# Kernel tuning notes

Hardware: AMD Instinct MI355X
Metric: run time of the kernel (lower is better)

## Reference

```python
import jax, jax.numpy as jnp
import numpy as np

B, T, H, U = 64, 4096, 256, 256


def setup_inputs() -> dict:
    key = jax.random.key(0)
    ks = jax.random.split(key, 8)
    s = 1.0 / np.sqrt(H)
    return {
        "query": jax.random.normal(ks[0], (B, H), dtype=jnp.float32),
        "values": jax.random.normal(ks[1], (B, T, H), dtype=jnp.float32),
        "W1": jax.random.normal(ks[2], (H, U), dtype=jnp.float32) * s,
        "b1": jnp.zeros((U,), dtype=jnp.float32),
        "W2": jax.random.normal(ks[3], (H, U), dtype=jnp.float32) * s,
        "b2": jnp.zeros((U,), dtype=jnp.float32),
        "V": jax.random.normal(ks[4], (U, 1), dtype=jnp.float32) * (1.0 / np.sqrt(U)),
        "bV": jnp.zeros((1,), dtype=jnp.float32),
    }


def reference(query, values, W1, b1, W2, b2, V, bV):
    # query: [B,H] -> [B,1,U]; values: [B,T,H] -> [B,T,U]
    q_proj = (query @ W1 + b1)[:, None, :]            # [B,1,U]
    v_proj = jnp.einsum('bth,hu->btu', values, W2) + b2  # [B,T,U]
    score = jnp.tanh(q_proj + v_proj) @ V + bV        # [B,T,1]
    attention_weights = jax.nn.softmax(score, axis=1)  # softmax over T
    context_vector = jnp.sum(attention_weights * values, axis=1)  # [B,H]
    return context_vector, attention_weights
```

## Files before the change

### kernel.cpp

```cpp
#include <hip/hip_runtime.h>
#include <stdint.h>

#define B_ 64
#define T_ 4096
#define H_ 256
#define U_ 256

typedef float f32x4 __attribute__((ext_vector_type(4)));
typedef short short8 __attribute__((ext_vector_type(8)));

__device__ __forceinline__ short bf16rne(float f) {
    uint32_t x = __builtin_bit_cast(uint32_t, f);
    return (short)((x + 0x7FFFu + ((x >> 16) & 1u)) >> 16);
}

__device__ __forceinline__ float fast_tanh(float x) {
    float e = __expf(2.0f * x);
    return 1.0f - 2.0f * __builtin_amdgcn_rcpf(e + 1.0f);
}

__global__ __launch_bounds__(256) void k_prep(const float* __restrict__ W2,
                                              uint16_t* __restrict__ w2t,
                                              const float* __restrict__ query,
                                              const float* __restrict__ W1,
                                              const float* __restrict__ b1,
                                              const float* __restrict__ b2,
                                              float* __restrict__ qpc) {
    if (blockIdx.x < 256) {
        int idx = blockIdx.x * 256 + threadIdx.x;
        int h = idx >> 8;
        int u = idx & 255;
        w2t[u * 256 + h] = (uint16_t)bf16rne(W2[idx]);
    } else {
        __shared__ float qrow[H_];
        int b = blockIdx.x - 256, u = threadIdx.x;
        qrow[u] = query[b * H_ + u];
        __syncthreads();
        float acc = b1[u] + b2[u];
#pragma unroll 8
        for (int h = 0; h < H_; ++h) acc += qrow[h] * W1[h * U_ + u];
        qpc[b * U_ + u] = acc;
    }
}

#define TR 32
#define NT 8
__global__ __launch_bounds__(512, 2) void k_main(const float* __restrict__ values,
                                                 const uint16_t* __restrict__ w2t,
                                                 const float* __restrict__ qpc,
                                                 const float* __restrict__ V,
                                                 float* __restrict__ score,
                                                 float* __restrict__ part_O,
                                                 float* __restrict__ part_s) {
    __shared__ __align__(16) char Ab[TR * 512];
    __shared__ float red[TR][9];
    __shared__ float Ored[TR][16][16];
    __shared__ float sred[TR];

    const int tid = threadIdx.x;
    const int wg = blockIdx.x;
    const int b = wg >> 4;
    const int chunk = (wg & 15) * (NT * TR);

    const int w = tid >> 6;
    const int l = tid & 63;
    const int c = l & 15;
    const int g = l >> 4;

    short8 afr[2][8];
#pragma unroll
    for (int s = 0; s < 2; ++s) {
        const uint16_t* ap = w2t + (size_t)(w * 32 + s * 16 + c) * 256 + g * 8;
#pragma unroll
        for (int ks = 0; ks < 8; ++ks) afr[s][ks] = *(const short8*)(ap + ks * 32);
    }
    float qv[2][4], vv[2][4];
#pragma unroll
    for (int s = 0; s < 2; ++s)
#pragma unroll
        for (int r = 0; r < 4; ++r) {
            int u = w * 32 + s * 16 + g * 4 + r;
            qv[s][r] = qpc[b * U_ + u];
            vv[s][r] = V[u];
        }

    const float* vbase = values + (size_t)b * T_ * H_;
    const int srow = tid >> 4;
    const int q = tid & 15;
    const int sswz = (srow & 7) << 4;
    char* wr0 = Ab + srow * 512 + ((q * 16) ^ sswz);
    char* wr1 = Ab + srow * 512 + ((q * 16 + 256) ^ sswz);
    const float* sbase = vbase + (size_t)srow * H_ + q * 8;

    f32x4 vt[3][4];
    float Oacc[16];
#pragma unroll
    for (int j = 0; j < 16; ++j) Oacc[j] = 0.f;
    float sacc = 0.f;

    {
        const float* nb0 = sbase + (size_t)chunk * H_;
        vt[0][0] = *(const f32x4*)(nb0);       vt[0][1] = *(const f32x4*)(nb0 + 4);
        vt[0][2] = *(const f32x4*)(nb0 + 128); vt[0][3] = *(const f32x4*)(nb0 + 132);
        const float* nb1 = sbase + (size_t)(chunk + TR) * H_;
        vt[1][0] = *(const f32x4*)(nb1);       vt[1][1] = *(const f32x4*)(nb1 + 4);
        vt[1][2] = *(const f32x4*)(nb1 + 128); vt[1][3] = *(const f32x4*)(nb1 + 132);
    }

#pragma unroll
    for (int t = 0; t < NT; ++t) {
        const int cs = t % 3;
        const int os = (t + 2) % 3;
        __syncthreads();
        {
            short8 s0, s1;
            s0[0] = bf16rne(vt[cs][0][0]); s0[1] = bf16rne(vt[cs][0][1]);
            s0[2] = bf16rne(vt[cs][0][2]); s0[3] = bf16rne(vt[cs][0][3]);
            s0[4] = bf16rne(vt[cs][1][0]); s0[5] = bf16rne(vt[cs][1][1]);
            s0[6] = bf16rne(vt[cs][1][2]); s0[7] = bf16rne(vt[cs][1][3]);
            s1[0] = bf16rne(vt[cs][2][0]); s1[1] = bf16rne(vt[cs][2][1]);
            s1[2] = bf16rne(vt[cs][2][2]); s1[3] = bf16rne(vt[cs][2][3]);
            s1[4] = bf16rne(vt[cs][3][0]); s1[5] = bf16rne(vt[cs][3][1]);
            s1[6] = bf16rne(vt[cs][3][2]); s1[7] = bf16rne(vt[cs][3][3]);
            *(short8*)wr0 = s0;
            *(short8*)wr1 = s1;
        }
        if (t > 0) {
            float ssum = 0.f;
#pragma unroll
            for (int j = 0; j < 8; ++j) ssum += red[srow][j];
            float wgt = __expf(ssum);
            if (q == 0) {
                sacc += wgt;
                score[(size_t)b * T_ + chunk + (t - 1) * TR + srow] = ssum;
            }
#pragma unroll
            for (int vj = 0; vj < 4; ++vj)
#pragma unroll
                for (int j = 0; j < 4; ++j)
                    Oacc[vj * 4 + j] += wgt * vt[os][vj][j];
        }
        if (t + 2 < NT) {
            const float* nb = sbase + (size_t)(chunk + (t + 2) * TR) * H_;
            vt[os][0] = *(const f32x4*)(nb);       vt[os][1] = *(const f32x4*)(nb + 4);
            vt[os][2] = *(const f32x4*)(nb + 128); vt[os][3] = *(const f32x4*)(nb + 132);
        }
        __syncthreads();
#pragma unroll
        for (int sub = 0; sub < 2; ++sub) {
            const char* rp = Ab + (sub * 16 + c) * 512;
            const int swz = (c & 7) << 4;
            f32x4 acc0 = (f32x4)(0.0f);
            f32x4 acc1 = (f32x4)(0.0f);
#pragma unroll
            for (int ks = 0; ks < 8; ++ks) {
                short8 bf = *(const short8*)(rp + ((ks * 64 + g * 16) ^ swz));
                acc0 = __builtin_amdgcn_mfma_f32_16x16x32_bf16(afr[0][ks], bf, acc0, 0, 0, 0);
                acc1 = __builtin_amdgcn_mfma_f32_16x16x32_bf16(afr[1][ks], bf, acc1, 0, 0, 0);
            }
            float p = 0.f;
#pragma unroll
            for (int r = 0; r < 4; ++r) {
                p += fast_tanh(acc0[r] + qv[0][r]) * vv[0][r];
                p += fast_tanh(acc1[r] + qv[1][r]) * vv[1][r];
            }
            p += __shfl_xor(p, 16, 64);
            p += __shfl_xor(p, 32, 64);
            if (g == 0) red[sub * 16 + c][w] = p;
        }
    }
    __syncthreads();
    {
        const int fs = (NT - 1) % 3;
        float ssum = 0.f;
#pragma unroll
        for (int j = 0; j < 8; ++j) ssum += red[srow][j];
        float wgt = __expf(ssum);
        if (q == 0) {
            sacc += wgt;
            score[(size_t)b * T_ + chunk + (NT - 1) * TR + srow] = ssum;
        }
#pragma unroll
        for (int vj = 0; vj < 4; ++vj)
#pragma unroll
            for (int j = 0; j < 4; ++j)
                Oacc[vj * 4 + j] += wgt * vt[fs][vj][j];
    }
#pragma unroll
    for (int j = 0; j < 16; ++j) Ored[srow][q][j] = Oacc[j];
    if (q == 0) sred[srow] = sacc;
    __syncthreads();
    if (tid < 256) {
        int col = tid;
        int qq, jj;
        if (col < 128) { qq = col >> 3; jj = col & 7; }
        else           { qq = (col - 128) >> 3; jj = 8 + (col & 7); }
        float o = 0.f;
#pragma unroll
        for (int s = 0; s < TR; ++s) o += Ored[s][qq][jj];
        part_O[(size_t)wg * 256 + col] = o;
    }
    if (tid == 0) {
        float sb = 0.f;
#pragma unroll
        for (int s = 0; s < TR; ++s) sb += sred[s];
        part_s[wg] = sb;
    }
}

__global__ __launch_bounds__(256) void k_fin(const float* __restrict__ part_O,
                                             const float* __restrict__ part_s,
                                             const float* __restrict__ score,
                                             float* __restrict__ ctx,
                                             float* __restrict__ weights) {
    int b = blockIdx.x;
    int col = threadIdx.x;
    float sb = 0.f;
#pragma unroll
    for (int ch = 0; ch < 16; ++ch) sb += part_s[b * 16 + ch];
    float o = 0.f;
#pragma unroll
    for (int ch = 0; ch < 16; ++ch) o += part_O[(size_t)(b * 16 + ch) * 256 + col];
    float inv = 1.0f / sb;
    ctx[b * H_ + col] = o * inv;
#pragma unroll
    for (int i = 0; i < 16; ++i) {
        float s = score[(size_t)b * T_ + col + i * 256];
        weights[(size_t)b * T_ + col + i * 256] = __expf(s) * inv;
    }
}

extern "C" void kernel_launch(void* const* d_in, const int* in_sizes, int n_in,
                              void* d_out, int out_size, void* d_ws, size_t ws_size,
                              hipStream_t stream) {
    const float* query  = (const float*)d_in[0];
    const float* values = (const float*)d_in[1];
    const float* W1     = (const float*)d_in[2];
    const float* b1     = (const float*)d_in[3];
    const float* W2     = (const float*)d_in[4];
    const float* b2     = (const float*)d_in[5];
    const float* V      = (const float*)d_in[6];

    float* out = (float*)d_out;
    float* ctx = out;
    float* weights = out + B_ * H_;

    char* ws = (char*)d_ws;
    uint16_t* w2t   = (uint16_t*)ws;
    float* qpc      = (float*)(ws + 131072);
    float* scorebuf = (float*)(ws + 131072 + 65536);
    float* part_O   = (float*)(ws + 131072 + 65536 + 1048576);
    float* part_s   = (float*)(ws + 131072 + 65536 + 2097152);

    k_prep<<<dim3(320), dim3(256), 0, stream>>>(W2, w2t, query, W1, b1, b2, qpc);
    k_main<<<dim3(1024), dim3(512), 0, stream>>>(values, w2t, qpc, V, scorebuf,
                                                 part_O, part_s);
    k_fin<<<dim3(64), dim3(256), 0, stream>>>(part_O, part_s, scorebuf, ctx, weights);
}
```

Measured before the change: 93.42 us.

## Double-buffer LDS tiles, remap value loads per wave, widen finalize grid

Measured after the change: 126.7 us. 35.6% more time.

```diff
diff --git a/kernel.cpp b/kernel.cpp
--- a/kernel.cpp
+++ b/kernel.cpp
@@ -8,6 +8,7 @@
 
 typedef float f32x4 __attribute__((ext_vector_type(4)));
 typedef short short8 __attribute__((ext_vector_type(8)));
+typedef short short4v __attribute__((ext_vector_type(4)));
 
 __device__ __forceinline__ short bf16rne(float f) {
     uint32_t x = __builtin_bit_cast(uint32_t, f);
@@ -52,10 +53,10 @@
                                                  float* __restrict__ score,
                                                  float* __restrict__ part_O,
                                                  float* __restrict__ part_s) {
-    __shared__ __align__(16) char Ab[TR * 512];
-    __shared__ float red[TR][9];
-    __shared__ float Ored[TR][16][16];
-    __shared__ float sred[TR];
+    __shared__ __align__(16) char Ab[2][TR * 512];
+    __shared__ float red[2][TR][12];
+    __shared__ float Ored[8][256];
+    __shared__ float sred[8];
 
     const int tid = threadIdx.x;
     const int wg = blockIdx.x;
@@ -84,71 +85,71 @@
             vv[s][r] = V[u];
         }
 
-    const float* vbase = values + (size_t)b * T_ * H_;
-    const int srow = tid >> 4;
-    const int q = tid & 15;
-    const int sswz = (srow & 7) << 4;
-    char* wr0 = Ab + srow * 512 + ((q * 16) ^ sswz);
-    char* wr1 = Ab + srow * 512 + ((q * 16 + 256) ^ sswz);
-    const float* sbase = vbase + (size_t)srow * H_ + q * 8;
+    const float* vbase = values + (size_t)b * T_ * H_ + (size_t)chunk * H_;
+    const int sswz = (l * 8) ^ (w << 4);
 
     f32x4 vt[3][4];
-    float Oacc[16];
-#pragma unroll
-    for (int j = 0; j < 16; ++j) Oacc[j] = 0.f;
+    float Oacc[4] = {0.f, 0.f, 0.f, 0.f};
     float sacc = 0.f;
 
-    {
-        const float* nb0 = sbase + (size_t)chunk * H_;
-        vt[0][0] = *(const f32x4*)(nb0);       vt[0][1] = *(const f32x4*)(nb0 + 4);
-        vt[0][2] = *(const f32x4*)(nb0 + 128); vt[0][3] = *(const f32x4*)(nb0 + 132);
-        const float* nb1 = sbase + (size_t)(chunk + TR) * H_;
-        vt[1][0] = *(const f32x4*)(nb1);       vt[1][1] = *(const f32x4*)(nb1 + 4);
-        vt[1][2] = *(const f32x4*)(nb1 + 128); vt[1][3] = *(const f32x4*)(nb1 + 132);
+#pragma unroll
+    for (int j = 0; j < 4; ++j) {
+        vt[0][j] = *(const f32x4*)(vbase + j * 2048 + w * 256 + l * 4);
+        vt[1][j] = *(const f32x4*)(vbase + 8192 + j * 2048 + w * 256 + l * 4);
+    }
+#pragma unroll
+    for (int j = 0; j < 4; ++j) {
+        short4v s4;
+        s4[0] = bf16rne(vt[0][j][0]); s4[1] = bf16rne(vt[0][j][1]);
+        s4[2] = bf16rne(vt[0][j][2]); s4[3] = bf16rne(vt[0][j][3]);
+        *(short4v*)(Ab[0] + (j * 8 + w) * 512 + sswz) = s4;
     }
 
 #pragma unroll
     for (int t = 0; t < NT; ++t) {
-        const int cs = t % 3;
-        const int os = (t + 2) % 3;
         __syncthreads();
-        {
-            short8 s0, s1;
-            s0[0] = bf16rne(vt[cs][0][0]); s0[1] = bf16rne(vt[cs][0][1]);
-            s0[2] = bf16rne(vt[cs][0][2]); s0[3] = bf16rne(vt[cs][0][3]);
-            s0[4] = bf16rne(vt[cs][1][0]); s0[5] = bf16rne(vt[cs][1][1]);
-            s0[6] = bf16rne(vt[cs][1][2]); s0[7] = bf16rne(vt[cs][1][3]);
-            s1[0] = bf16rne(vt[cs][2][0]); s1[1] = bf16rne(vt[cs][2][1]);
-            s1[2] = bf16rne(vt[cs][2][2]); s1[3] = bf16rne(vt[cs][2][3]);
-            s1[4] = bf16rne(vt[cs][3][0]); s1[5] = bf16rne(vt[cs][3][1]);
-            s1[6] = bf16rne(vt[cs][3][2]); s1[7] = bf16rne(vt[cs][3][3]);
-            *(short8*)wr0 = s0;
-            *(short8*)wr1 = s1;
-        }
         if (t > 0) {
-            float ssum = 0.f;
-#pragma unroll
-            for (int j = 0; j < 8; ++j) ssum += red[srow][j];
-            float wgt = __expf(ssum);
-            if (q == 0) {
-                sacc += wgt;
-                score[(size_t)b * T_ + chunk + (t - 1) * TR + srow] = ssum;
-            }
-#pragma unroll
-            for (int vj = 0; vj < 4; ++vj)
-#pragma unroll
-                for (int j = 0; j < 4; ++j)
-                    Oacc[vj * 4 + j] += wgt * vt[os][vj][j];
+            const int os = (t + 2) % 3;
+            float p = 0.f;
+            if (l < 4) {
+                const float* rr = &red[(t - 1) & 1][l * 8 + w][0];
+                f32x4 r0 = *(const f32x4*)(rr);
+                f32x4 r1 = *(const f32x4*)(rr + 4);
+                float ssum = (r0[0] + r0[1] + r0[2] + r0[3]) +
+                             (r1[0] + r1[1] + r1[2] + r1[3]);
+                p = __expf(ssum);
+                sacc += p;
+                score[(size_t)b * T_ + chunk + (t - 1) * TR + l * 8 + w] = ssum;
+            }
+#pragma unroll
+            for (int j = 0; j < 4; ++j) {
+                float wgt = __shfl(p, j, 64);
+                Oacc[0] += wgt * vt[os][j][0];
+                Oacc[1] += wgt * vt[os][j][1];
+                Oacc[2] += wgt * vt[os][j][2];
+                Oacc[3] += wgt * vt[os][j][3];
+            }
         }
         if (t + 2 < NT) {
-            const float* nb = sbase + (size_t)(chunk + (t + 2) * TR) * H_;
-            vt[os][0] = *(const f32x4*)(nb);       vt[os][1] = *(const f32x4*)(nb + 4);
-            vt[os][2] = *(const f32x4*)(nb + 128); vt[os][3] = *(const f32x4*)(nb + 132);
-        }
-        __syncthreads();
+            const int ns = (t + 2) % 3;
+            const float* nb = vbase + (size_t)(t + 2) * 8192;
+#pragma unroll
+            for (int j = 0; j < 4; ++j)
+                vt[ns][j] = *(const f32x4*)(nb + j * 2048 + w * 256 + l * 4);
+        }
+        if (t + 1 < NT) {
+            const int cs = (t + 1) % 3;
+#pragma unroll
+            for (int j = 0; j < 4; ++j) {
+                short4v s4;
+                s4[0] = bf16rne(vt[cs][j][0]); s4[1] = bf16rne(vt[cs][j][1]);
+                s4[2] = bf16rne(vt[cs][j][2]); s4[3] = bf16rne(vt[cs][j][3]);
+                *(short4v*)(Ab[(t + 1) & 1] + (j * 8 + w) * 512 + sswz) = s4;
+            }
+        }
 #pragma unroll
         for (int sub = 0; sub < 2; ++sub) {
-            const char* rp = Ab + (sub * 16 + c) * 512;
+            const char* rp = Ab[t & 1] + (sub * 16 + c) * 512;
             const int swz = (c & 7) << 4;
             f32x4 acc0 = (f32x4)(0.0f);
             f32x4 acc1 = (f32x4)(0.0f);
@@ -166,44 +167,47 @@
             }
             p += __shfl_xor(p, 16, 64);
             p += __shfl_xor(p, 32, 64);
-            if (g == 0) red[sub * 16 + c][w] = p;
+            if (g == 0) red[t & 1][sub * 16 + c][w] = p;
         }
     }
     __syncthreads();
     {
         const int fs = (NT - 1) % 3;
-        float ssum = 0.f;
-#pragma unroll
-        for (int j = 0; j < 8; ++j) ssum += red[srow][j];
-        float wgt = __expf(ssum);
-        if (q == 0) {
-            sacc += wgt;
-            score[(size_t)b * T_ + chunk + (NT - 1) * TR + srow] = ssum;
-        }
-#pragma unroll
-        for (int vj = 0; vj < 4; ++vj)
-#pragma unroll
-            for (int j = 0; j < 4; ++j)
-                Oacc[vj * 4 + j] += wgt * vt[fs][vj][j];
-    }
-#pragma unroll
-    for (int j = 0; j < 16; ++j) Ored[srow][q][j] = Oacc[j];
-    if (q == 0) sred[srow] = sacc;
+        float p = 0.f;
+        if (l < 4) {
+            const float* rr = &red[(NT - 1) & 1][l * 8 + w][0];
+            f32x4 r0 = *(const f32x4*)(rr);
+            f32x4 r1 = *(const f32x4*)(rr + 4);
+            float ssum = (r0[0] + r0[1] + r0[2] + r0[3]) +
+                         (r1[0] + r1[1] + r1[2] + r1[3]);
+            p = __expf(ssum);
+            sacc += p;
+            score[(size_t)b * T_ + chunk + (NT - 1) * TR + l * 8 + w] = ssum;
+        }
+#pragma unroll
+        for (int j = 0; j < 4; ++j) {
+            float wgt = __shfl(p, j, 64);
+            Oacc[0] += wgt * vt[fs][j][0];
+            Oacc[1] += wgt * vt[fs][j][1];
+            Oacc[2] += wgt * vt[fs][j][2];
+            Oacc[3] += wgt * vt[fs][j][3];
+        }
+    }
+    *(f32x4*)(&Ored[w][l * 4]) = *(f32x4*)Oacc;
+    sacc += __shfl_xor(sacc, 1, 64);
+    sacc += __shfl_xor(sacc, 2, 64);
+    if (l == 0) sred[w] = sacc;
     __syncthreads();
     if (tid < 256) {
-        int col = tid;
-        int qq, jj;
-        if (col < 128) { qq = col >> 3; jj = col & 7; }
-        else           { qq = (col - 128) >> 3; jj = 8 + (col & 7); }
         float o = 0.f;
 #pragma unroll
-        for (int s = 0; s < TR; ++s) o += Ored[s][qq][jj];
-        part_O[(size_t)wg * 256 + col] = o;
+        for (int j = 0; j < 8; ++j) o += Ored[j][tid];
+        part_O[(size_t)wg * 256 + tid] = o;
     }
     if (tid == 0) {
         float sb = 0.f;
 #pragma unroll
-        for (int s = 0; s < TR; ++s) sb += sred[s];
+        for (int j = 0; j < 8; ++j) sb += sred[j];
         part_s[wg] = sb;
     }
 }
@@ -213,20 +217,24 @@
                                              const float* __restrict__ score,
                                              float* __restrict__ ctx,
                                              float* __restrict__ weights) {
-    int b = blockIdx.x;
+    int b = blockIdx.x >> 3;
+    int j = blockIdx.x & 7;
     int col = threadIdx.x;
     float sb = 0.f;
 #pragma unroll
     for (int ch = 0; ch < 16; ++ch) sb += part_s[b * 16 + ch];
-    float o = 0.f;
-#pragma unroll
-    for (int ch = 0; ch < 16; ++ch) o += part_O[(size_t)(b * 16 + ch) * 256 + col];
     float inv = 1.0f / sb;
-    ctx[b * H_ + col] = o * inv;
-#pragma unroll
-    for (int i = 0; i < 16; ++i) {
-        float s = score[(size_t)b * T_ + col + i * 256];
-        weights[(size_t)b * T_ + col + i * 256] = __expf(s) * inv;
+    if (j == 0) {
+        float o = 0.f;
+#pragma unroll
+        for (int ch = 0; ch < 16; ++ch) o += part_O[(size_t)(b * 16 + ch) * 256 + col];
+        ctx[b * H_ + col] = o * inv;
+    }
+#pragma unroll
+    for (int i = 0; i < 2; ++i) {
+        int idx = j * 512 + i * 256 + col;
+        float s = score[(size_t)b * T_ + idx];
+        weights[(size_t)b * T_ + idx] = __expf(s) * inv;
     }
 }
 
@@ -255,5 +263,5 @@
     k_prep<<<dim3(320), dim3(256), 0, stream>>>(W2, w2t, query, W1, b1, b2, qpc);
     k_main<<<dim3(1024), dim3(512), 0, stream>>>(values, w2t, qpc, V, scorebuf,
                                                  part_O, part_s);
-    k_fin<<<dim3(64), dim3(256), 0, stream>>>(part_O, part_s, scorebuf, ctx, weights);
-}
+    k_fin<<<dim3(512), dim3(256), 0, stream>>>(part_O, part_s, scorebuf, ctx, weights);
+}
```
